# Kernel tuning notes

Measured on AMD Instinct MI355X. Metric: run time of the kernel, lower is better.

The kernel has to match this reference:

```python
import jax, jax.numpy as jnp
import numpy as np

H = 512          # hidden_size
OBS, PRED = 32, 32
T = OBS + PRED
N_OTHERS = 4096
MC = 4           # map_channels
NEMB = 10        # scene embedding vocab
MAP_HW = 256


def setup_inputs() -> dict:
    key = jax.random.key(0)
    ks = jax.random.split(key, 24)
    def rn(k, shape, scale=0.05):
        return jax.random.normal(k, shape, dtype=jnp.float32) * scale
    return {
        "target": rn(ks[0], (T, 1, 2), 1.0),
        "others": rn(ks[1], (OBS, N_OTHERS, 2), 1.0),
        "scene_map": jax.random.randint(ks[2], (MAP_HW, MAP_HW), 0, NEMB, dtype=jnp.int32),
        # scene branch params
        "emb": rn(ks[3], (NEMB, MC)),
        "conv1_w": rn(ks[4], (16, MC, 3, 3)),
        "conv1_b": rn(ks[5], (16,)),
        "conv2_w": rn(ks[6], (32, 16, 3, 3)),
        "conv2_b": rn(ks[7], (32,)),
        "scene_fc_w": rn(ks[8], (H, 32)),
        "scene_fc_b": rn(ks[9], (H,)),
        # shared LSTMCell params (PyTorch layout: gates i,f,g,o stacked)
        "w_ih": rn(ks[10], (4 * H, 2)),
        "w_hh": rn(ks[11], (4 * H, H)),
        "b_ih": rn(ks[12], (4 * H,)),
        "b_hh": rn(ks[13], (4 * H,)),
        # social attention params
        "wq": rn(ks[14], (H, H)), "bq": rn(ks[15], (H,)),
        "wk": rn(ks[16], (H, H)), "bk": rn(ks[17], (H,)),
        "wv": rn(ks[18], (H, H)), "bv": rn(ks[19], (H,)),
        # output layer
        "out_w": rn(ks[20], (2, H)), "out_b": rn(ks[21], (2,)),
    }


def _lstm_cell(x, h, c, w_ih, w_hh, b_ih, b_hh):
    # PyTorch LSTMCell: gates in order i, f, g, o
    gates = x @ w_ih.T + b_ih + h @ w_hh.T + b_hh
    i, f, g, o = jnp.split(gates, 4, axis=-1)
    c2 = jax.nn.sigmoid(f) * c + jax.nn.sigmoid(i) * jnp.tanh(g)
    return jax.nn.sigmoid(o) * jnp.tanh(c2), c2


def _scene_feature(scene_map, emb, c1w, c1b, c2w, c2b, fcw, fcb):
    # embedding -> NCHW -> conv3x3/relu x2 -> global avg pool -> fc
    x = emb[scene_map][None].transpose(0, 3, 1, 2)          # [1,MC,Hm,Wm]
    x = jax.lax.conv_general_dilated(x, c1w, (1, 1), 'SAME') + c1b[None, :, None, None]
    x = jax.nn.relu(x)
    x = jax.lax.conv_general_dilated(x, c2w, (1, 1), 'SAME') + c2b[None, :, None, None]
    x = jax.nn.relu(x)
    x = x.mean(axis=(2, 3))                                 # [1,32]
    return x @ fcw.T + fcb                                  # [1,H]


def reference(target, others, scene_map, emb, conv1_w, conv1_b, conv2_w, conv2_b,
              scene_fc_w, scene_fc_b, w_ih, w_hh, b_ih, b_hh,
              wq, bq, wk, bk, wv, bv, out_w, out_b):
    Tlen = target.shape[0]
    obs_len = others.shape[0]
    hdim = w_hh.shape[1]
    n_others = others.shape[1]
    # scene_map is constant across the loop -> compute once (identical math)
    scene_feat = _scene_feature(scene_map, emb, conv1_w, conv1_b, conv2_w, conv2_b,
                                scene_fc_w, scene_fc_b)    # [1,H]
    # others_pos at step t is others[min(t, obs_len-1)]
    idx = jnp.minimum(jnp.arange(Tlen), obs_len - 1)
    others_seq = others[idx]                                # [T,N,2]
    target_seq = target[:, 0:1, :]                          # [T,1,2] (teacher forcing, train=True)
    temperature = jnp.sqrt(jnp.asarray(wq.shape[0], jnp.float32))

    def step(carry, xs):
        ht, ct, ho, co = carry
        tp, op = xs
        ht, ct = _lstm_cell(tp, ht, ct, w_ih, w_hh, b_ih, b_hh)
        ho, co = _lstm_cell(op, ho, co, w_ih, w_hh, b_ih, b_hh)
        q = ht @ wq.T + bq                                  # [1,H]
        k = ho @ wk.T + bk                                  # [N,H]
        v = ho @ wv.T + bv                                  # [N,H]
        attn = jax.nn.softmax((q @ k.T) / temperature, axis=1)  # [1,N]
        social = attn @ v                                   # [1,H]
        out = (ht + social + scene_feat) @ out_w.T + out_b  # [1,2]
        return (ht, ct, ho, co), out

    z1 = jnp.zeros((1, hdim), jnp.float32)
    zN = jnp.zeros((n_others, hdim), jnp.float32)
    _, outs = jax.lax.scan(step, (z1, z1, zN, zN), (target_seq, others_seq))
    return outs                                             # [T,1,2]
```

## Files before the change

### kernel.cpp

```cpp
#include <hip/hip_runtime.h>
#include <hip/hip_bf16.h>


typedef __bf16 bf16x8 __attribute__((ext_vector_type(8)));
typedef float  f32x4  __attribute__((ext_vector_type(4)));

#define KD 512

__device__ __forceinline__ void gl_lds16(const void* g, void* l) {
  __builtin_amdgcn_global_load_lds(
      (const __attribute__((address_space(1))) void*)g,
      (__attribute__((address_space(3))) void*)l, 16, 0, 0);
}
__device__ __forceinline__ float sigm(float x) {
  return __builtin_amdgcn_rcpf(1.f + __expf(-x));
}
__device__ __forceinline__ float tanh_f(float x) {
  return 2.f * __builtin_amdgcn_rcpf(1.f + __expf(-2.f * x)) - 1.f;
}
__device__ __forceinline__ float sel4(f32x4 v, int i) {
  float a = (i & 1) ? v[1] : v[0];
  float b = (i & 1) ? v[3] : v[2];
  return (i & 2) ? b : a;
}
__device__ __forceinline__ float pick(int m, float o0, float o1, float o2, float o3) {
  float a = (m & 1) ? o1 : o0;
  float b = (m & 1) ? o3 : o2;
  return (m & 2) ? b : a;
}
__device__ __forceinline__ float agent_ldf(const float* p) {
  return __hip_atomic_load(p, __ATOMIC_RELAXED, __HIP_MEMORY_SCOPE_AGENT);
}
__device__ __forceinline__ void agent_stf(float* p, float v) {
  __hip_atomic_store(p, v, __ATOMIC_RELAXED, __HIP_MEMORY_SCOPE_AGENT);
}

struct SP {
  const unsigned short* Wp;
  unsigned short* A0; unsigned short* A1;
  __bf16* Zb0; __bf16* Zb1;
  float* q0; float* q1;
  __bf16* coB;
  float* ht;
  const float* biasz;
  const float4* bs4; const float4* w04; const float4* w14;
  const float* others; const float* target;
  const float* scene; const float* out_w; const float* out_b;
  float* part; unsigned int* cnt;
  float* out;
};

__device__ void do_gemm(const SP& P, int p, int bm, int bn)
{
  __shared__ __align__(16) char aLds[2][128 * 128 * 2];

  const int tid = threadIdx.x, wave = tid >> 6, lane = tid & 63;
  const unsigned short* A = (p & 1) ? P.A1 : P.A0;
  __bf16* An = (__bf16*)((p & 1) ? P.A0 : P.A1);
  __bf16* Zb = (p & 1) ? P.Zb1 : P.Zb0;
  float* qv  = (p & 1) ? P.q1 : P.q0;
  const int tin = (p + 1 < 31) ? (p + 1) : 31;
  const int tc  = (p + 1 < 63) ? (p + 1) : 63;
  const float* op = P.others + (size_t)tin * 8192;
  const float* tp = P.target + tc * 2;
  float* htn = P.ht + (size_t)(p + 1) * 512;

  const int m0 = bm * 128;
  const int l15 = lane & 15, lq = lane >> 4;

  int aRow[8], aOff[8], ldsOff[8];
#pragma unroll
  for (int j = 0; j < 8; ++j) {
    int chunk = j * 4 + wave;
    int r = chunk * 4 + (lane >> 4);
    int ch = lane & 15;
    aRow[j]   = m0 + r;
    aOff[j]   = (ch ^ (r & 15)) * 8;
    ldsOff[j] = chunk * 1024;
  }
  const unsigned short* bBase =
      P.Wp + (size_t)(bn * 16 + wave * 4) * 8192 + lq * 128 + l15 * 8;

  f32x4 acc[8][4];
#pragma unroll
  for (int i = 0; i < 8; ++i)
#pragma unroll
    for (int j = 0; j < 4; ++j) acc[i][j] = f32x4{0.f, 0.f, 0.f, 0.f};

  bf16x8 bCur[4], bNext[4], bNext2[4];

#pragma unroll
  for (int j = 0; j < 8; ++j)
    gl_lds16(A + (size_t)aRow[j] * KD + aOff[j], aLds[0] + ldsOff[j]);
#pragma unroll
  for (int nt = 0; nt < 4; ++nt) {
    bCur[nt]  = *(const bf16x8*)(bBase + nt * 8192);
    bNext[nt] = *(const bf16x8*)(bBase + nt * 8192 + 512);
  }
  __syncthreads();

#pragma unroll
  for (int kc = 0; kc < 16; ++kc) {
    const int it = kc >> 2, cc = kc & 3;
    if (cc == 0 && it < 3) {
      const int k1 = (it + 1) * 128;
#pragma unroll
      for (int j = 0; j < 8; ++j)
        gl_lds16(A + (size_t)aRow[j] * KD + k1 + aOff[j],
                 aLds[(it + 1) & 1] + ldsOff[j]);
    }
    if (kc + 2 < 16) {
#pragma unroll
      for (int nt = 0; nt < 4; ++nt)
        bNext2[nt] = *(const bf16x8*)(bBase + nt * 8192 + (kc + 2) * 512);
    }
    const char* buf = aLds[it & 1];
    bf16x8 af[8];
#pragma unroll
    for (int mt = 0; mt < 8; ++mt) {
      int row = mt * 16 + l15;
      int g = (cc * 4 + lq) ^ (row & 15);
      af[mt] = *(const bf16x8*)(buf + row * 256 + g * 16);
    }
#pragma unroll
    for (int mt = 0; mt < 8; ++mt)
#pragma unroll
      for (int nt = 0; nt < 4; ++nt)
        acc[mt][nt] = __builtin_amdgcn_mfma_f32_16x16x32_bf16(
            af[mt], bCur[nt], acc[mt][nt], 0, 0, 0);
#pragma unroll
    for (int nt = 0; nt < 4; ++nt) {
      bCur[nt] = bNext[nt];
      bNext[nt] = bNext2[nt];
    }
    if (cc == 3) __syncthreads();
  }

  const int rq = lq * 4;

  if (bn >= 12) {
    if (lq == 0) {
#pragma unroll
      for (int nt = 0; nt < 4; ++nt) {
        int qcol = (bn - 12) * 256 + wave * 64 + nt * 16 + l15;
        qv[qcol] = acc[0][nt][0] + P.biasz[1024 + qcol];
      }
    }
    return;
  }

  if (bn >= 8) {
    __bf16* zT = (__bf16*)aLds;
    const int zbase = (bn - 8) * 256;
    float bias[4];
#pragma unroll
    for (int nt = 0; nt < 4; ++nt)
      bias[nt] = P.biasz[zbase + wave * 64 + nt * 16 + l15];
#pragma unroll
    for (int mt = 0; mt < 8; ++mt) {
#pragma unroll
      for (int nt = 0; nt < 4; ++nt) {
        int ulocal = wave * 64 + nt * 16 + l15;
#pragma unroll
        for (int r = 0; r < 4; ++r) {
          int rloc = mt * 16 + rq + r;
          zT[rloc * 256 + ulocal] = (__bf16)(acc[mt][nt][r] + bias[nt]);
        }
      }
    }
    __syncthreads();
    const bf16x8* zc = (const bf16x8*)zT;
#pragma unroll
    for (int i = 0; i < 16; ++i) {
      int idx = i * 256 + tid;
      int rloc = idx >> 5, c8 = idx & 31;
      *(bf16x8*)(Zb + (size_t)(m0 + rloc) * 1024 + zbase + c8 * 8) = zc[idx];
    }
    return;
  }

  const int rho = lane & 3, usel = (lane >> 2) & 3;
  const int u0 = bn * 64 + wave * 16;
  float4 bsv[4], w0v[4], w1v[4];
  int uu[4];
#pragma unroll
  for (int nt = 0; nt < 4; ++nt) {
    uu[nt]  = u0 + nt * 4 + usel;
    bsv[nt] = P.bs4[uu[nt]];
    w0v[nt] = P.w04[uu[nt]];
    w1v[nt] = P.w14[uu[nt]];
  }

  if (bm < 32) {
    __bf16* hT = (__bf16*)aLds[0];
    __bf16* cT = (__bf16*)aLds[1];
#pragma unroll
    for (int mt = 0; mt < 8; ++mt) {
      int rloc = mt * 16 + rq + rho;
      int row  = m0 + rloc;
      float x0 = op[2 * row], x1 = op[2 * row + 1];
#pragma unroll
      for (int nt = 0; nt < 4; ++nt) {
        f32x4 v = acc[mt][nt];
        float own = sel4(v, rho);
        float r1  = __shfl_xor(sel4(v, rho ^ 1), 1, 64);
        float r2  = __shfl_xor(sel4(v, rho ^ 2), 2, 64);
        float r3  = __shfl_xor(sel4(v, rho ^ 3), 3, 64);
        float g0 = pick(rho,     own, r1, r2, r3);
        float g1 = pick(rho ^ 1, own, r1, r2, r3);
        float g2 = pick(rho ^ 2, own, r1, r2, r3);
        float g3 = pick(rho ^ 3, own, r1, r2, r3);
        float4 bs = bsv[nt], w0 = w0v[nt], w1 = w1v[nt];
        float p0 = g0 + bs.x + w0.x * x0 + w1.x * x1;
        float p1 = g1 + bs.y + w0.y * x0 + w1.y * x1;
        float p2 = g2 + bs.z + w0.z * x0 + w1.z * x1;
        float p3 = g3 + bs.w + w0.w * x0 + w1.w * x1;
        int u = uu[nt];
        size_t ci = (size_t)row * 512 + u;
        float c_old = (float)P.coB[ci];
        float ii = sigm(p0), ff = sigm(p1), gg = tanh_f(p2), oo = sigm(p3);
        float cn = ff * c_old + ii * gg;
        float h  = oo * tanh_f(cn);
        int ulocal = u - bn * 64;
        hT[rloc * 64 + ulocal] = (__bf16)h;
        cT[rloc * 64 + ulocal] = (__bf16)cn;
      }
    }
    __syncthreads();
    const bf16x8* hc = (const bf16x8*)hT;
    const bf16x8* cc = (const bf16x8*)cT;
#pragma unroll
    for (int i = 0; i < 4; ++i) {
      int idx = i * 256 + tid;
      int rloc = idx >> 3, c8 = idx & 7;
      size_t base = (size_t)(m0 + rloc) * 512 + bn * 64 + c8 * 8;
      *(bf16x8*)(An + base)    = hc[idx];
      *(bf16x8*)(P.coB + base) = cc[idx];
    }
    return;
  }

#pragma unroll
  for (int mt = 0; mt < 8; ++mt) {
    int row = m0 + mt * 16 + rq + rho;
    bool act = row <= 4096;
    float x0 = 0.f, x1 = 0.f;
    if (act) {
      if (row < 4096) { x0 = op[2 * row]; x1 = op[2 * row + 1]; }
      else            { x0 = tp[0];       x1 = tp[1]; }
    }
#pragma unroll
    for (int nt = 0; nt < 4; ++nt) {
      f32x4 v = acc[mt][nt];
      float own = sel4(v, rho);
      float r1  = __shfl_xor(sel4(v, rho ^ 1), 1, 64);
      float r2  = __shfl_xor(sel4(v, rho ^ 2), 2, 64);
      float r3  = __shfl_xor(sel4(v, rho ^ 3), 3, 64);
      float g0 = pick(rho,     own, r1, r2, r3);
      float g1 = pick(rho ^ 1, own, r1, r2, r3);
      float g2 = pick(rho ^ 2, own, r1, r2, r3);
      float g3 = pick(rho ^ 3, own, r1, r2, r3);
      if (act) {
        float4 bs = bsv[nt], w0 = w0v[nt], w1 = w1v[nt];
        float p0 = g0 + bs.x + w0.x * x0 + w1.x * x1;
        float p1 = g1 + bs.y + w0.y * x0 + w1.y * x1;
        float p2 = g2 + bs.z + w0.z * x0 + w1.z * x1;
        float p3 = g3 + bs.w + w0.w * x0 + w1.w * x1;
        int u = uu[nt];
        size_t ci = (size_t)row * 512 + u;
        float c_old = (float)P.coB[ci];
        float ii = sigm(p0), ff = sigm(p1), gg = tanh_f(p2), oo = sigm(p3);
        float cn = ff * c_old + ii * gg;
        float h  = oo * tanh_f(cn);
        P.coB[ci] = (__bf16)cn;
        An[ci] = (__bf16)h;
        if (row == 4096) htn[u] = h;
      }
    }
  }
}

__device__ void do_att(const SP& P, int p, int b)
{
  __shared__ __align__(16) float qs[512];
  __shared__ float red[256];
  __shared__ float red2[256];
  __shared__ float es[64];
  __shared__ unsigned int sOld;
  const int t = threadIdx.x;
  const __bf16* Zb = (p & 1) ? P.Zb1 : P.Zb0;
  const float* qv  = (p & 1) ? P.q1 : P.q0;
  const float* ht  = P.ht + (size_t)p * 512;

  for (int c = t; c < 512; c += 256) qs[c] = qv[c];
  __syncthreads();

  const int r0 = b * 64, rl = t >> 2, p4 = t & 3;
  const bf16x8* krow = (const bf16x8*)(Zb + (size_t)(r0 + rl) * 1024);
  float a = 0.f;
  for (int i = p4; i < 64; i += 4) {
    bf16x8 kk = krow[i];
    const float* qq = qs + i * 8;
#pragma unroll
    for (int j = 0; j < 8; ++j) a += (float)kk[j] * qq[j];
  }
  red[t] = a;
  __syncthreads();
  if (t < 64)
    es[t] = __expf((red[4 * t] + red[4 * t + 1] + red[4 * t + 2] + red[4 * t + 3]) *
                   0.04419417382415922f);
  __syncthreads();

  float s0 = 0.f, s1 = 0.f;
  for (int r = 0; r < 64; ++r) {
    const __bf16* vr = Zb + (size_t)(r0 + r) * 1024 + 512;
    float e = es[r];
    s0 += e * (float)vr[t];
    s1 += e * (float)vr[t + 256];
  }
  agent_stf(&P.part[b * 513 + t], s0);
  agent_stf(&P.part[b * 513 + 256 + t], s1);
  if (t == 0) {
    float se = 0.f;
#pragma unroll
    for (int r = 0; r < 64; ++r) se += es[r];
    agent_stf(&P.part[b * 513 + 512], se);
  }
  asm volatile("s_waitcnt vmcnt(0) lgkmcnt(0)" ::: "memory");
  __syncthreads();
  if (t == 0) sOld = atomicAdd(P.cnt, 1u);
  __syncthreads();
  if (sOld == 63) {
    float s = 0.f, s2 = 0.f, se = 0.f;
    for (int bb = 0; bb < 64; ++bb) {
      s  += agent_ldf(&P.part[bb * 513 + t]);
      s2 += agent_ldf(&P.part[bb * 513 + 256 + t]);
      se += agent_ldf(&P.part[bb * 513 + 512]);
    }
    float inv = 1.f / se;
    float va = ht[t] + s * inv + P.scene[t];
    float vb = ht[t + 256] + s2 * inv + P.scene[t + 256];
    red[t]  = va * P.out_w[t]       + vb * P.out_w[t + 256];
    red2[t] = va * P.out_w[512 + t] + vb * P.out_w[768 + t];
    __syncthreads();
    for (int st = 128; st > 0; st >>= 1) {
      if (t < st) { red[t] += red[t + st]; red2[t] += red2[t + st]; }
      __syncthreads();
    }
    if (t == 0) {
      P.out[2 * p]     = red[0]  + P.out_b[0];
      P.out[2 * p + 1] = red2[0] + P.out_b[1];
      *P.cnt = 0;
    }
  }
}

__global__ __launch_bounds__(256, 2) void step_kernel(SP P, int p)
{
  const int xcd  = blockIdx.x & 7;
  const int slot = blockIdx.x >> 3;
  if (slot < 56) {
    const int r = xcd >> 1, c = xcd & 1;
    const int bm = 8 * r + slot / 7;
    const int j  = 2 * (slot % 7) + c;
    if (j < 12) {
      do_gemm(P, p, bm, j);
    } else {
      if (p >= 1) do_att(P, p - 1, 2 * bm + (j - 12));
    }
  } else {
    const int ti = (slot == 56) ? xcd : (8 + xcd);
    const int bn = (ti < 8) ? ti : (12 + (ti - 8));
    do_gemm(P, p, 32, bn);
  }
}

__global__ __launch_bounds__(256) void att_step(SP P, int p) {
  do_att(P, p, blockIdx.x);
}

__global__ __launch_bounds__(256) void init_state(
    const float* __restrict__ others0, const float* __restrict__ target0,
    const float* __restrict__ w_ih, const float* __restrict__ b_ih,
    const float* __restrict__ b_hh,
    __bf16* __restrict__ coB, __bf16* __restrict__ A0, float* __restrict__ ht0,
    unsigned int* __restrict__ cnt)
{
  int g = blockIdx.x * 256 + threadIdx.x;
  if (g == 0) *cnt = 0u;
  if (g >= 4097 * 512) return;
  int r = g >> 9, j = g & 511;
  float x0, x1;
  if (r < 4096) { x0 = others0[2 * r]; x1 = others0[2 * r + 1]; }
  else          { x0 = target0[0];     x1 = target0[1]; }
  float pre[4];
#pragma unroll
  for (int gg = 0; gg < 4; ++gg) {
    int n = gg * 512 + j;
    pre[gg] = b_ih[n] + b_hh[n] + w_ih[2 * n] * x0 + w_ih[2 * n + 1] * x1;
  }
  float cn = sigm(pre[0]) * tanh_f(pre[2]);
  float h  = sigm(pre[3]) * tanh_f(cn);
  coB[g] = (__bf16)cn;
  A0[g] = (__bf16)h;
  if (r == 4096) ht0[j] = h;
}

__global__ __launch_bounds__(256) void pack_w(
    const float* __restrict__ w_hh, const float* __restrict__ wk,
    const float* __restrict__ wv,   const float* __restrict__ wq,
    __bf16* __restrict__ Wp)
{
  int o = blockIdx.x * 256 + threadIdx.x;
  int j = o & 7, nn = (o >> 3) & 15, kg = (o >> 7) & 63, ntg = o >> 13;
  int n = ntg * 16 + nn, k = kg * 8 + j;
  float v;
  if (n < 2048)      { int u = n >> 2, g = n & 3; v = w_hh[(g * 512 + u) * 512 + k]; }
  else if (n < 2560) v = wk[(n - 2048) * 512 + k];
  else if (n < 3072) v = wv[(n - 2560) * 512 + k];
  else               v = wq[(n - 3072) * 512 + k];
  Wp[o] = (__bf16)v;
}

__global__ __launch_bounds__(256) void pack_misc(
    const float* __restrict__ b_ih, const float* __restrict__ b_hh,
    const float* __restrict__ w_ih,
    const float* __restrict__ bk, const float* __restrict__ bv,
    const float* __restrict__ bq,
    float* __restrict__ bs, float* __restrict__ w0, float* __restrict__ w1,
    float* __restrict__ biasz)
{
  int i = blockIdx.x * 256 + threadIdx.x;
  if (i < 2048) {
    int u = i >> 2, g = i & 3, n = g * 512 + u;
    bs[i] = b_ih[n] + b_hh[n];
    w0[i] = w_ih[2 * n];
    w1[i] = w_ih[2 * n + 1];
  } else if (i < 2048 + 1536) {
    int z = i - 2048;
    biasz[z] = (z < 512) ? bk[z] : (z < 1024 ? bv[z - 512] : bq[z - 1024]);
  }
}

__global__ __launch_bounds__(256) void scene1_kernel(
    const int* __restrict__ map, const float* __restrict__ emb,
    const float* __restrict__ w1, const float* __restrict__ b1,
    float* __restrict__ out1)
{
  __shared__ float wl[576];
  __shared__ float bl[16];
  const int t = threadIdx.x;
  for (int i = t; i < 576; i += 256) wl[i] = w1[i];
  if (t < 16) bl[t] = b1[t];
  __syncthreads();
  const int y = blockIdx.x, x = t;
  float nb[4][9];
#pragma unroll
  for (int dy = 0; dy < 3; ++dy)
#pragma unroll
    for (int dx = 0; dx < 3; ++dx) {
      int yy = y + dy - 1, xx = x + dx - 1;
      bool ok = (yy >= 0 && yy < 256 && xx >= 0 && xx < 256);
      int m = ok ? map[yy * 256 + xx] : 0;
#pragma unroll
      for (int c = 0; c < 4; ++c)
        nb[c][dy * 3 + dx] = ok ? emb[m * 4 + c] : 0.f;
    }
  for (int oc = 0; oc < 16; ++oc) {
    float a = bl[oc];
#pragma unroll
    for (int c = 0; c < 4; ++c)
#pragma unroll
      for (int k = 0; k < 9; ++k) a += wl[(oc * 4 + c) * 9 + k] * nb[c][k];
    out1[oc * 65536 + y * 256 + x] = fmaxf(a, 0.f);
  }
}

__global__ __launch_bounds__(256) void scene2_kernel(
    const float* __restrict__ out1, const float* __restrict__ w2,
    const float* __restrict__ b2, float* __restrict__ rowpart)
{
  __shared__ float wl[1152];
  __shared__ float lds4[4 * 8];
  const int t = threadIdx.x;
  const int y = blockIdx.x & 255, ocg = blockIdx.x >> 8;
  for (int i = t; i < 1152; i += 256) wl[i] = w2[ocg * 1152 + i];
  __syncthreads();
  const int x = t;
  float acc[8];
#pragma unroll
  for (int o = 0; o < 8; ++o) acc[o] = b2[ocg * 8 + o];
  for (int ic = 0; ic < 16; ++ic) {
    float nb[9];
#pragma unroll
    for (int dy = 0; dy < 3; ++dy)
#pragma unroll
      for (int dx = 0; dx < 3; ++dx) {
        int yy = y + dy - 1, xx = x + dx - 1;
        bool ok = (yy >= 0 && yy < 256 && xx >= 0 && xx < 256);
        nb[dy * 3 + dx] = ok ? out1[ic * 65536 + yy * 256 + xx] : 0.f;
      }
#pragma unroll
    for (int o = 0; o < 8; ++o) {
      const float* w = &wl[(o * 16 + ic) * 9];
#pragma unroll
      for (int k = 0; k < 9; ++k) acc[o] += w[k] * nb[k];
    }
  }
  const int wave = t >> 6, lane = t & 63;
#pragma unroll
  for (int o = 0; o < 8; ++o) {
    float v = fmaxf(acc[o], 0.f);
#pragma unroll
    for (int m = 1; m < 64; m <<= 1) v += __shfl_xor(v, m, 64);
    if (lane == 0) lds4[wave * 8 + o] = v;
  }
  __syncthreads();
  if (t < 8)
    rowpart[y * 32 + ocg * 8 + t] = lds4[t] + lds4[8 + t] + lds4[16 + t] + lds4[24 + t];
}

__global__ __launch_bounds__(512) void scene3_kernel(
    const float* __restrict__ rowpart, const float* __restrict__ fcw,
    const float* __restrict__ fcb, float* __restrict__ scene)
{
  __shared__ float mean[32];
  const int t = threadIdx.x;
  if (t < 32) {
    float s = 0.f;
    for (int y = 0; y < 256; ++y) s += rowpart[y * 32 + t];
    mean[t] = s * (1.f / 65536.f);
  }
  __syncthreads();
  float a = fcb[t];
#pragma unroll
  for (int c = 0; c < 32; ++c) a += mean[c] * fcw[t * 32 + c];
  scene[t] = a;
}

extern "C" void kernel_launch(void* const* d_in, const int* in_sizes, int n_in,
                              void* d_out, int out_size, void* d_ws, size_t ws_size,
                              hipStream_t stream) {
  const float* target    = (const float*)d_in[0];
  const float* others    = (const float*)d_in[1];
  const int*   scene_map = (const int*)d_in[2];
  const float* emb       = (const float*)d_in[3];
  const float* c1w       = (const float*)d_in[4];
  const float* c1b       = (const float*)d_in[5];
  const float* c2w       = (const float*)d_in[6];
  const float* c2b       = (const float*)d_in[7];
  const float* fcw       = (const float*)d_in[8];
  const float* fcb       = (const float*)d_in[9];
  const float* w_ih      = (const float*)d_in[10];
  const float* w_hh      = (const float*)d_in[11];
  const float* b_ih      = (const float*)d_in[12];
  const float* b_hh      = (const float*)d_in[13];
  const float* wq        = (const float*)d_in[14];
  const float* bq        = (const float*)d_in[15];
  const float* wk        = (const float*)d_in[16];
  const float* bk        = (const float*)d_in[17];
  const float* wv        = (const float*)d_in[18];
  const float* bv        = (const float*)d_in[19];
  const float* out_w     = (const float*)d_in[20];
  const float* out_b     = (const float*)d_in[21];
  float* out = (float*)d_out;

  char* ws = (char*)d_ws;
  size_t off = 0;
  auto alloc = [&](size_t bytes) { size_t o = off; off += (bytes + 255) & ~(size_t)255; return o; };
  __bf16* Zb0   = (__bf16*)(ws + alloc((size_t)4096 * 1024 * 2));
  __bf16* Zb1   = (__bf16*)(ws + alloc((size_t)4096 * 1024 * 2));
  float*  q0    = (float*)(ws + alloc(512 * 4));
  float*  q1    = (float*)(ws + alloc(512 * 4));
  __bf16* Wp    = (__bf16*)(ws + alloc((size_t)1835008 * 2));
  __bf16* A0    = (__bf16*)(ws + alloc((size_t)4224 * 512 * 2));
  __bf16* A1    = (__bf16*)(ws + alloc((size_t)4224 * 512 * 2));
  __bf16* coB   = (__bf16*)(ws + alloc((size_t)4224 * 512 * 2));
  float*  ht    = (float*)(ws + alloc((size_t)65 * 512 * 4));
  float*  scene = (float*)(ws + alloc(2048));
  float*  part  = (float*)(ws + alloc(64 * 513 * 4));
  unsigned int* cnt = (unsigned int*)(ws + alloc(256));
  float*  bs    = (float*)(ws + alloc(2048 * 4));
  float*  w0p   = (float*)(ws + alloc(2048 * 4));
  float*  w1p   = (float*)(ws + alloc(2048 * 4));
  float*  biasz = (float*)(ws + alloc(1536 * 4));
  float*  out1  = (float*)(ws + alloc((size_t)16 * 65536 * 4));
  float*  rowp  = (float*)(ws + alloc(256 * 32 * 4));

  pack_w<<<7168, 256, 0, stream>>>(w_hh, wk, wv, wq, Wp);
  pack_misc<<<14, 256, 0, stream>>>(b_ih, b_hh, w_ih, bk, bv, bq, bs, w0p, w1p, biasz);
  scene1_kernel<<<256, 256, 0, stream>>>(scene_map, emb, c1w, c1b, out1);
  scene2_kernel<<<1024, 256, 0, stream>>>(out1, c2w, c2b, rowp);
  scene3_kernel<<<1, 512, 0, stream>>>(rowp, fcw, fcb, scene);
  init_state<<<8194, 256, 0, stream>>>(others, target, w_ih, b_ih, b_hh, coB, A0, ht, cnt);

  SP hp;
  hp.Wp = (const unsigned short*)Wp;
  hp.A0 = (unsigned short*)A0; hp.A1 = (unsigned short*)A1;
  hp.Zb0 = Zb0; hp.Zb1 = Zb1;
  hp.q0 = q0; hp.q1 = q1;
  hp.coB = coB; hp.ht = ht;
  hp.biasz = biasz;
  hp.bs4 = (const float4*)bs; hp.w04 = (const float4*)w0p; hp.w14 = (const float4*)w1p;
  hp.others = others; hp.target = target;
  hp.scene = scene; hp.out_w = out_w; hp.out_b = out_b;
  hp.part = part; hp.cnt = cnt;
  hp.out = out;

  for (int p = 0; p < 64; ++p)
    step_kernel<<<458, 256, 0, stream>>>(hp, p);
  att_step<<<64, 256, 0, stream>>>(hp, 63);
}
```

Before: 1.717 ms.

## Triple-buffer A tiles in LDS with smaller K chunks and vmcnt-based waits

The A-operand staging changes from two 128-wide K buffers to three 64-wide K buffers, prefetched two stages ahead, with a partial s_waitcnt vmcnt plus barrier instead of full __syncthreads. The LDS swizzle is reworked for 128-byte rows. Total LDS shrinks from 64KB to 48KB, so the Z epilogue now transposes and stores in two halves with extra barriers. The aim is to overlap global-to-LDS loads with MFMA work and lower LDS use, at the cost of more barriers and a hand-counted vmcnt that must stay correct.

```diff
diff --git a/kernel.cpp b/kernel.cpp
--- a/kernel.cpp
+++ b/kernel.cpp
@@ -52,7 +52,7 @@
 
 __device__ void do_gemm(const SP& P, int p, int bm, int bn)
 {
-  __shared__ __align__(16) char aLds[2][128 * 128 * 2];
+  __shared__ __align__(16) char aLds[3][128 * 64 * 2];
 
   const int tid = threadIdx.x, wave = tid >> 6, lane = tid & 63;
   const unsigned short* A = (p & 1) ? P.A1 : P.A0;
@@ -68,14 +68,12 @@
   const int m0 = bm * 128;
   const int l15 = lane & 15, lq = lane >> 4;
 
-  int aRow[8], aOff[8], ldsOff[8];
-#pragma unroll
-  for (int j = 0; j < 8; ++j) {
+  int aRow[4], aOff[4], ldsOff[4];
+#pragma unroll
+  for (int j = 0; j < 4; ++j) {
     int chunk = j * 4 + wave;
-    int r = chunk * 4 + (lane >> 4);
-    int ch = lane & 15;
-    aRow[j]   = m0 + r;
-    aOff[j]   = (ch ^ (r & 15)) * 8;
+    aRow[j]   = m0 + chunk * 8 + (lane >> 3);
+    aOff[j]   = ((lane & 7) ^ (lane >> 3)) * 8;
     ldsOff[j] = chunk * 1024;
   }
   const unsigned short* bBase =
@@ -90,8 +88,11 @@
   bf16x8 bCur[4], bNext[4], bNext2[4];
 
 #pragma unroll
-  for (int j = 0; j < 8; ++j)
-    gl_lds16(A + (size_t)aRow[j] * KD + aOff[j], aLds[0] + ldsOff[j]);
+  for (int j = 0; j < 4; ++j)
+    gl_lds16(A + (size_t)aRow[j] * KD + 0 * 64 + aOff[j], aLds[0] + ldsOff[j]);
+#pragma unroll
+  for (int j = 0; j < 4; ++j)
+    gl_lds16(A + (size_t)aRow[j] * KD + 1 * 64 + aOff[j], aLds[1] + ldsOff[j]);
 #pragma unroll
   for (int nt = 0; nt < 4; ++nt) {
     bCur[nt]  = *(const bf16x8*)(bBase + nt * 8192);
@@ -100,41 +101,49 @@
   __syncthreads();
 
 #pragma unroll
-  for (int kc = 0; kc < 16; ++kc) {
-    const int it = kc >> 2, cc = kc & 3;
-    if (cc == 0 && it < 3) {
-      const int k1 = (it + 1) * 128;
-#pragma unroll
-      for (int j = 0; j < 8; ++j)
-        gl_lds16(A + (size_t)aRow[j] * KD + k1 + aOff[j],
-                 aLds[(it + 1) & 1] + ldsOff[j]);
-    }
-    if (kc + 2 < 16) {
-#pragma unroll
-      for (int nt = 0; nt < 4; ++nt)
-        bNext2[nt] = *(const bf16x8*)(bBase + nt * 8192 + (kc + 2) * 512);
-    }
-    const char* buf = aLds[it & 1];
-    bf16x8 af[8];
-#pragma unroll
-    for (int mt = 0; mt < 8; ++mt) {
-      int row = mt * 16 + l15;
-      int g = (cc * 4 + lq) ^ (row & 15);
-      af[mt] = *(const bf16x8*)(buf + row * 256 + g * 16);
-    }
-#pragma unroll
-    for (int mt = 0; mt < 8; ++mt)
-#pragma unroll
-      for (int nt = 0; nt < 4; ++nt)
-        acc[mt][nt] = __builtin_amdgcn_mfma_f32_16x16x32_bf16(
-            af[mt], bCur[nt], acc[mt][nt], 0, 0, 0);
-#pragma unroll
-    for (int nt = 0; nt < 4; ++nt) {
-      bCur[nt] = bNext[nt];
-      bNext[nt] = bNext2[nt];
-    }
-    if (cc == 3) __syncthreads();
-  }
+  for (int it = 0; it < 8; ++it) {
+    if (it > 0) {
+      asm volatile("s_waitcnt vmcnt(8)" ::: "memory");
+      __builtin_amdgcn_s_barrier();
+      __builtin_amdgcn_sched_barrier(0);
+    }
+    if (it + 2 < 8) {
+      const int k2 = (it + 2) * 64;
+      char* dst = aLds[(it + 2) % 3];
+#pragma unroll
+      for (int j = 0; j < 4; ++j)
+        gl_lds16(A + (size_t)aRow[j] * KD + k2 + aOff[j], dst + ldsOff[j]);
+    }
+    const char* buf = aLds[it % 3];
+#pragma unroll
+    for (int cc = 0; cc < 2; ++cc) {
+      const int kc = it * 2 + cc;
+      if (kc + 2 < 16) {
+#pragma unroll
+        for (int nt = 0; nt < 4; ++nt)
+          bNext2[nt] = *(const bf16x8*)(bBase + nt * 8192 + (kc + 2) * 512);
+      }
+      bf16x8 af[8];
+#pragma unroll
+      for (int mt = 0; mt < 8; ++mt) {
+        int row = mt * 16 + l15;
+        int s = (cc * 4 + lq) ^ (row & 7);
+        af[mt] = *(const bf16x8*)(buf + row * 128 + s * 16);
+      }
+#pragma unroll
+      for (int mt = 0; mt < 8; ++mt)
+#pragma unroll
+        for (int nt = 0; nt < 4; ++nt)
+          acc[mt][nt] = __builtin_amdgcn_mfma_f32_16x16x32_bf16(
+              af[mt], bCur[nt], acc[mt][nt], 0, 0, 0);
+#pragma unroll
+      for (int nt = 0; nt < 4; ++nt) {
+        bCur[nt] = bNext[nt];
+        bNext[nt] = bNext2[nt];
+      }
+    }
+  }
+  __syncthreads();
 
   const int rq = lq * 4;
 
@@ -157,24 +166,29 @@
     for (int nt = 0; nt < 4; ++nt)
       bias[nt] = P.biasz[zbase + wave * 64 + nt * 16 + l15];
 #pragma unroll
-    for (int mt = 0; mt < 8; ++mt) {
-#pragma unroll
-      for (int nt = 0; nt < 4; ++nt) {
-        int ulocal = wave * 64 + nt * 16 + l15;
-#pragma unroll
-        for (int r = 0; r < 4; ++r) {
-          int rloc = mt * 16 + rq + r;
-          zT[rloc * 256 + ulocal] = (__bf16)(acc[mt][nt][r] + bias[nt]);
+    for (int half = 0; half < 2; ++half) {
+#pragma unroll
+      for (int mt2 = 0; mt2 < 4; ++mt2) {
+        int mt = half * 4 + mt2;
+#pragma unroll
+        for (int nt = 0; nt < 4; ++nt) {
+          int ulocal = wave * 64 + nt * 16 + l15;
+#pragma unroll
+          for (int r = 0; r < 4; ++r) {
+            int rloc = mt2 * 16 + rq + r;
+            zT[rloc * 256 + ulocal] = (__bf16)(acc[mt][nt][r] + bias[nt]);
+          }
         }
       }
-    }
-    __syncthreads();
-    const bf16x8* zc = (const bf16x8*)zT;
-#pragma unroll
-    for (int i = 0; i < 16; ++i) {
-      int idx = i * 256 + tid;
-      int rloc = idx >> 5, c8 = idx & 31;
-      *(bf16x8*)(Zb + (size_t)(m0 + rloc) * 1024 + zbase + c8 * 8) = zc[idx];
+      __syncthreads();
+      const bf16x8* zc = (const bf16x8*)zT;
+#pragma unroll
+      for (int i = 0; i < 8; ++i) {
+        int idx = i * 256 + tid;
+        int rloc = idx >> 5, c8 = idx & 31;
+        *(bf16x8*)(Zb + (size_t)(m0 + half * 64 + rloc) * 1024 + zbase + c8 * 8) = zc[idx];
+      }
+      __syncthreads();
     }
     return;
   }
```

After: 1.751 ms. Within noise of the previous version (+2.0%).
